# Performance work log

Measured on AMD Instinct MI355X. Metric: run time of the kernel, lower is better.

## Reference

```python
import jax, jax.numpy as jnp
from jax import lax
import numpy as np

DIM = 384
H = W = 32
B = 32
HALF = DIM // 2


def _parc(x, pe, w, b, axis):
    """Global circular depthwise conv along `axis` (2=H, 3=W). w: (C,1,kh,kw)."""
    x = x + pe
    k = x.shape[axis]
    if axis == 2:
        x_cat = jnp.concatenate([x, x[:, :, : k - 1, :]], axis=2)
    else:
        x_cat = jnp.concatenate([x, x[:, :, :, : k - 1]], axis=3)
    out = lax.conv_general_dilated(
        x_cat, w, window_strides=(1, 1), padding='VALID',
        dimension_numbers=('NCHW', 'OIHW', 'NCHW'),
        feature_group_count=x.shape[1])
    return out + b[None, :, None, None]


def setup_inputs() -> dict:
    key = jax.random.key(0)
    ks = jax.random.split(key, 12)
    std = 0.02
    return {
        'x': jax.random.normal(ks[0], (B, DIM, H, W), jnp.float32),
        'pe_h': std * jax.random.normal(ks[1], (1, HALF, H, 1), jnp.float32),
        'w_h': std * jax.random.normal(ks[2], (HALF, 1, H, 1), jnp.float32),
        'b_h': jnp.zeros((HALF,), jnp.float32),
        'pe_w': std * jax.random.normal(ks[3], (1, HALF, 1, W), jnp.float32),
        'w_w': std * jax.random.normal(ks[4], (HALF, 1, 1, W), jnp.float32),
        'b_w': jnp.zeros((HALF,), jnp.float32),
        'ln_w': jnp.ones((DIM,), jnp.float32),
        'ln_b': jnp.zeros((DIM,), jnp.float32),
        'w1': std * jax.random.normal(ks[5], (DIM, 4 * DIM), jnp.float32),
        'b1': jnp.zeros((4 * DIM,), jnp.float32),
        'w2': std * jax.random.normal(ks[6], (4 * DIM, DIM), jnp.float32),
        'b2': jnp.zeros((DIM,), jnp.float32),
        'gamma': 1e-6 * jnp.ones((DIM,), jnp.float32),
    }


def reference(x, pe_h, w_h, b_h, pe_w, w_w, b_w, ln_w, ln_b, w1, b1, w2, b2, gamma):
    inp = x
    half = x.shape[1] // 2
    x_h = _parc(x[:, :half], pe_h, w_h, b_h, axis=2)
    x_w = _parc(x[:, half:], pe_w, w_w, b_w, axis=3)
    y = jnp.concatenate([x_h, x_w], axis=1).transpose(0, 2, 3, 1)  # NHWC
    # LayerNorm over channels (eps=1e-6)
    mu = y.mean(-1, keepdims=True)
    var = ((y - mu) ** 2).mean(-1, keepdims=True)
    y = (y - mu) / jnp.sqrt(var + 1e-6) * ln_w + ln_b
    # inverted MLP: dim -> 4*dim -> dim with exact GELU
    y = jax.nn.gelu(jnp.dot(y, w1) + b1, approximate=False)
    y = jnp.dot(y, w2) + b2
    y = gamma * y
    return inp + y.transpose(0, 3, 1, 2)
```

## Files before the change

kernel.cpp:

```cpp
#include <hip/hip_runtime.h>


typedef __attribute__((ext_vector_type(8))) short short8;
typedef __attribute__((ext_vector_type(4))) float f32x4;
typedef __attribute__((ext_vector_type(16))) float f32x16;
typedef __attribute__((ext_vector_type(4))) int int4v;
typedef __attribute__((ext_vector_type(8))) int i32x8;

__device__ __forceinline__ float bf2f(unsigned short u) {
  union { unsigned int i; float f; } v; v.i = ((unsigned int)u) << 16; return v.f;
}
__device__ __forceinline__ unsigned short f2bf(float f) {
  union { float f; unsigned int i; } v; v.f = f;
  unsigned int r = v.i + 0x7FFFu + ((v.i >> 16) & 1u);
  return (unsigned short)(r >> 16);
}

#if defined(__has_builtin)
#if __has_builtin(__builtin_amdgcn_global_load_lds)
#define HAS_GLL 1
#endif
#endif
#ifndef HAS_GLL
#define HAS_GLL 0
#endif

#if HAS_GLL
__device__ __forceinline__ void gload16(const void* g, void* l) {
  __builtin_amdgcn_global_load_lds((const __attribute__((address_space(1))) void*)g,
                                   (__attribute__((address_space(3))) void*)l, 16, 0, 0);
}
#else
__device__ __forceinline__ void gload16(const void* g, void* l) {
  *(f32x4*)l = *(const f32x4*)g;
}
#endif

template <int N>
__device__ __forceinline__ void wait_vm() {
  asm volatile("s_waitcnt vmcnt(%0)" :: "n"(N) : "memory");
}
__device__ __forceinline__ void barrier_raw() {
  __builtin_amdgcn_s_barrier();
  __builtin_amdgcn_sched_barrier(0);
}

__device__ __forceinline__ float fast_gelu(float h) {
  const float e = __builtin_amdgcn_exp2f(-2.4554005f * h);
  return h * __builtin_amdgcn_rcpf(1.f + e);
}

__device__ __forceinline__ int pk4(float a, float b, float c, float d) {
  int r = __builtin_amdgcn_cvt_pk_fp8_f32(a, b, 0, false);
  return __builtin_amdgcn_cvt_pk_fp8_f32(c, d, r, true);
}

#define SCL1 0x7F7F7F7F

__global__ __launch_bounds__(256) void pack_kernel(
    const float* __restrict__ w1, const float* __restrict__ w2,
    char* __restrict__ w1p, char* __restrict__ w2p) {
  const int t = threadIdx.x;
  const int bid = blockIdx.x;
  float v[64];
  if (bid < 36) {
    const int kt = bid % 6, hg = bid / 6;
    const int h = hg * 256 + t;
    #pragma unroll
    for (int k = 0; k < 64; ++k) v[k] = w1[(size_t)(kt * 64 + k) * 1536 + h];
    const int swz = (h >> 1) & 3;
    char* rowp = w1p + ((size_t)(kt * 1536 + h)) * 64;
    #pragma unroll
    for (int k0 = 0; k0 < 64; k0 += 4) {
      const int chunk = (k0 >> 4) ^ swz;
      *(int*)(rowp + chunk * 16 + (k0 & 12)) = pk4(v[k0], v[k0 + 1], v[k0 + 2], v[k0 + 3]);
    }
  } else {
    const int kt = bid - 36;
    for (int c = t; c < 384; c += 256) {
      #pragma unroll
      for (int k = 0; k < 64; ++k) v[k] = w2[(size_t)(kt * 64 + k) * 384 + c];
      const int swz = (c >> 1) & 3;
      char* rowp = w2p + ((size_t)(kt * 384 + c)) * 64;
      #pragma unroll
      for (int k0 = 0; k0 < 64; k0 += 4) {
        const int chunk = (k0 >> 4) ^ swz;
        *(int*)(rowp + chunk * 16 + (k0 & 12)) = pk4(v[k0], v[k0 + 1], v[k0 + 2], v[k0 + 3]);
      }
    }
  }
}

__global__ __launch_bounds__(256) void conv_kernel(
    const float* __restrict__ x,
    const float* __restrict__ pe_h, const float* __restrict__ w_h, const float* __restrict__ b_h,
    const float* __restrict__ pe_w, const float* __restrict__ w_w, const float* __restrict__ b_w,
    unsigned short* __restrict__ convout) {
  __shared__ float wt_s[8][32], pe_s[8][32], pc_s[8][32];
  const int t = threadIdx.x;
  const int bid = blockIdx.x;
  const int b = bid / 48, g = bid % 48;
  const int c0 = g << 3;
  const bool ish = (c0 < 192);
  const int cl = t >> 5, q = t & 31;
  {
    const int c = c0 + cl;
    if (ish) { wt_s[cl][q] = w_h[(c << 5) + q];           pe_s[cl][q] = pe_h[(c << 5) + q]; }
    else     { const int cc = c - 192;
               wt_s[cl][q] = w_w[(cc << 5) + q];          pe_s[cl][q] = pe_w[(cc << 5) + q]; }
  }
  __syncthreads();
  {
    float s = ish ? b_h[c0 + cl] : b_w[c0 + cl - 192];
    #pragma unroll
    for (int i = 0; i < 32; ++i) s += pe_s[cl][(q + i) & 31] * wt_s[cl][i];
    pc_s[cl][q] = s;
  }
  __syncthreads();
  const float* xp = x + ((size_t)(b * 384 + c0 + cl) << 10);
  float col[32];
  if (ish) {
    #pragma unroll
    for (int j = 0; j < 32; ++j) col[j] = xp[(j << 5) + q];
  } else {
    const float* rp = xp + (q << 5);
    #pragma unroll
    for (int j4 = 0; j4 < 8; ++j4) {
      f32x4 v = *(const f32x4*)&rp[j4 << 2];
      col[j4 * 4 + 0] = v[0]; col[j4 * 4 + 1] = v[1];
      col[j4 * 4 + 2] = v[2]; col[j4 * 4 + 3] = v[3];
    }
  }
  float wr[32];
  #pragma unroll
  for (int i = 0; i < 32; ++i) wr[i] = wt_s[cl][i];
  float o[32];
  #pragma unroll
  for (int oo = 0; oo < 32; ++oo) o[oo] = pc_s[cl][oo];
  #pragma unroll
  for (int i = 0; i < 32; ++i)
    #pragma unroll
    for (int oo = 0; oo < 32; ++oo)
      o[oo] = fmaf(col[(oo + i) & 31], wr[i], o[oo]);
  unsigned short* op = convout + ((size_t)(b * 384 + c0 + cl) << 10);
  if (ish) {
    #pragma unroll
    for (int oo = 0; oo < 32; ++oo) op[(oo << 5) + q] = f2bf(o[oo]);
  } else {
    #pragma unroll
    for (int j8 = 0; j8 < 4; ++j8) {
      short8 p;
      #pragma unroll
      for (int j = 0; j < 8; ++j) p[j] = (short)f2bf(o[j8 * 8 + j]);
      *(short8*)&op[(q << 5) + j8 * 8] = p;
    }
  }
}

__global__ __launch_bounds__(256) void ln_stats_kernel(
    const unsigned short* __restrict__ conv,
    float* __restrict__ mu, float* __restrict__ rs) {
  __shared__ float sums[4][64], sqs[4][64];
  const int tid = threadIdx.x;
  const int lane = tid & 63;
  const int w = tid >> 6;
  const int px = blockIdx.x * 64 + lane;
  const int b = px >> 10, hw = px & 1023;
  const unsigned short* cp = conv + (((size_t)(b * 384 + w * 96)) << 10) + hw;
  float s = 0.f, ss = 0.f;
  #pragma unroll 8
  for (int k = 0; k < 96; ++k) {
    float v = bf2f(cp[(size_t)k << 10]);
    s += v; ss = fmaf(v, v, ss);
  }
  sums[w][lane] = s; sqs[w][lane] = ss;
  __syncthreads();
  if (tid < 64) {
    const float st = sums[0][tid] + sums[1][tid] + sums[2][tid] + sums[3][tid];
    const float sst = sqs[0][tid] + sqs[1][tid] + sqs[2][tid] + sqs[3][tid];
    const float m = st * (1.f / 384.f);
    const float var = sst * (1.f / 384.f) - m * m;
    mu[blockIdx.x * 64 + tid] = m;
    rs[blockIdx.x * 64 + tid] = rsqrtf(var + 1e-6f);
  }
}

__global__ __launch_bounds__(256) void ln_pack_kernel(
    const unsigned short* __restrict__ conv,
    const float* __restrict__ mu, const float* __restrict__ rs,
    char* __restrict__ ylnp,
    const float* __restrict__ ln_w, const float* __restrict__ ln_b) {
  __shared__ float lw[64], lb[64];
  const int kt = blockIdx.y;
  const int t = threadIdx.x;
  if (t < 64) { lw[t] = ln_w[kt * 64 + t]; lb[t] = ln_b[kt * 64 + t]; }
  __syncthreads();
  const int px = blockIdx.x * 256 + t;
  const int b = px >> 10, hw = px & 1023;
  const unsigned short* cp = conv + (((size_t)(b * 384 + kt * 64)) << 10) + hw;
  const float m = mu[px], r = rs[px];
  float ov[64];
  #pragma unroll
  for (int k = 0; k < 64; ++k) {
    const float v = bf2f(cp[(size_t)k << 10]);
    ov[k] = (v - m) * r * lw[k] + lb[k];
  }
  const int swz = (px >> 1) & 3;
  char* rowp = ylnp + ((size_t)(kt * 32768 + px)) * 64;
  #pragma unroll
  for (int q = 0; q < 4; ++q) {
    int4v d;
    d[0] = pk4(ov[q * 16 + 0],  ov[q * 16 + 1],  ov[q * 16 + 2],  ov[q * 16 + 3]);
    d[1] = pk4(ov[q * 16 + 4],  ov[q * 16 + 5],  ov[q * 16 + 6],  ov[q * 16 + 7]);
    d[2] = pk4(ov[q * 16 + 8],  ov[q * 16 + 9],  ov[q * 16 + 10], ov[q * 16 + 11]);
    d[3] = pk4(ov[q * 16 + 12], ov[q * 16 + 13], ov[q * 16 + 14], ov[q * 16 + 15]);
    *(int4v*)(rowp + ((q ^ swz) << 4)) = d;
  }
}

template <int EPI, int KDIM, int AROWS>
__global__ __launch_bounds__(256, 3) void gemm_kernel(
    const char* __restrict__ Ab, const char* __restrict__ Bb,
    char* __restrict__ Hout8, const float* __restrict__ bias,
    const float* __restrict__ gamma, const float* __restrict__ xres,
    float* __restrict__ out, int px0, int bstride, int boff, int hstride,
    int nwg, int nx) {
  extern __shared__ char lds[];
  constexpr int BM = 128, BN = 128;
  constexpr int NB = 3, DEPTH = 2;
  constexpr int NT = KDIM / 64;
  constexpr int SLOT = (BM + BN) * 64;
  constexpr int CH = 4;
  const int tid = threadIdx.x;
  const int lane = tid & 63;
  const int wid = tid >> 6;
  const int wm = wid >> 1, wn = wid & 1;
  const int lane31 = lane & 31;
  const int kh = lane >> 5;
  const int bid = blockIdx.x;
  const int q = nwg >> 3, r = nwg & 7;
  const int xcd = bid & 7, idx = bid >> 3;
  const int lg = (xcd < r ? xcd * (q + 1) : r * (q + 1) + (xcd - r) * q) + idx;
  const int xb = lg % nx, yb = lg / nx;
  const int arow0 = xb * BM;
  const int brow0 = yb * BN;

  f32x16 acc[2][2] = {};

  int aoff[2][2], boffl[2][2];
  #pragma unroll
  for (int m = 0; m < 2; ++m) {
    const int row = wm * 64 + m * 32 + lane31;
    const int s = (row >> 1) & 3;
    aoff[m][0] = row * 64 + (((2 * kh + 0) ^ s) << 4);
    aoff[m][1] = row * 64 + (((2 * kh + 1) ^ s) << 4);
  }
  #pragma unroll
  for (int n = 0; n < 2; ++n) {
    const int row = wn * 64 + n * 32 + lane31;
    const int s = (row >> 1) & 3;
    boffl[n][0] = BM * 64 + row * 64 + (((2 * kh + 0) ^ s) << 4);
    boffl[n][1] = BM * 64 + row * 64 + (((2 * kh + 1) ^ s) << 4);
  }

  auto stage = [&](int tile) {
    char* sl = lds + (size_t)(tile % NB) * SLOT;
    #pragma unroll
    for (int i = 0; i < 2; ++i) {
      const int c = i * 256 + tid;
      const int row = c >> 2, ch = c & 3;
      gload16(Ab + ((size_t)(tile * AROWS + arow0 + row)) * 64 + (ch << 4),
              sl + c * 16);
    }
    #pragma unroll
    for (int i = 0; i < 2; ++i) {
      const int c = i * 256 + tid;
      const int row = c >> 2, ch = c & 3;
      gload16(Bb + ((size_t)tile * bstride + boff + brow0 + row) * 64 + (ch << 4),
              sl + (BM * 4 + c) * 16);
    }
  };

  auto step = [&](int t, int stage_tile) {
    const char* slp = lds + (size_t)(t % NB) * SLOT;
    i32x8 av[2], bv[2];
    #pragma unroll
    for (int m = 0; m < 2; ++m) {
      int4v p0 = *(const int4v*)(slp + aoff[m][0]);
      int4v p1 = *(const int4v*)(slp + aoff[m][1]);
      av[m][0] = p0[0]; av[m][1] = p0[1]; av[m][2] = p0[2]; av[m][3] = p0[3];
      av[m][4] = p1[0]; av[m][5] = p1[1]; av[m][6] = p1[2]; av[m][7] = p1[3];
    }
    #pragma unroll
    for (int n = 0; n < 2; ++n) {
      int4v p0 = *(const int4v*)(slp + boffl[n][0]);
      int4v p1 = *(const int4v*)(slp + boffl[n][1]);
      bv[n][0] = p0[0]; bv[n][1] = p0[1]; bv[n][2] = p0[2]; bv[n][3] = p0[3];
      bv[n][4] = p1[0]; bv[n][5] = p1[1]; bv[n][6] = p1[2]; bv[n][7] = p1[3];
    }
    if (stage_tile >= 0) stage(stage_tile);
    __builtin_amdgcn_s_setprio(1);
    #pragma unroll
    for (int m = 0; m < 2; ++m)
      #pragma unroll
      for (int n = 0; n < 2; ++n)
        acc[m][n] = __builtin_amdgcn_mfma_scale_f32_32x32x64_f8f6f4(
            av[m], bv[n], acc[m][n], 0, 0, 0, SCL1, 0, SCL1);
    __builtin_amdgcn_s_setprio(0);
  };

  #pragma unroll
  for (int d = 0; d < DEPTH; ++d) stage(d);
  wait_vm<CH * (DEPTH - 1)>();
  barrier_raw();

  #pragma unroll 3
  for (int t = 0; t < NT - DEPTH; ++t) {
    step(t, t + DEPTH);
    wait_vm<CH * (DEPTH - 1)>();
    barrier_raw();
  }
  step(NT - 2, -1);
  wait_vm<0>();
  barrier_raw();
  step(NT - 1, -1);

  if (EPI == 0) {
    const int kt = (arow0 + wm * 64) >> 6;
    #pragma unroll
    for (int m = 0; m < 2; ++m) {
      #pragma unroll
      for (int G = 0; G < 4; ++G) {
        const int bytepos = m * 32 + 8 * G + 4 * kh;
        const int hg = arow0 + wm * 64 + bytepos;
        const float b0 = bias[hg + 0], b1v = bias[hg + 1];
        const float b2v = bias[hg + 2], b3v = bias[hg + 3];
        const int chunk = bytepos >> 4, sub = bytepos & 15;
        #pragma unroll
        for (int n = 0; n < 2; ++n) {
          const int px = brow0 + wn * 64 + n * 32 + lane31;
          const int d = pk4(fast_gelu(acc[m][n][4 * G + 0] + b0),
                            fast_gelu(acc[m][n][4 * G + 1] + b1v),
                            fast_gelu(acc[m][n][4 * G + 2] + b2v),
                            fast_gelu(acc[m][n][4 * G + 3] + b3v));
          const int pchunk = chunk ^ ((px >> 1) & 3);
          *(int*)(Hout8 + ((size_t)(kt * hstride + px)) * 64 + pchunk * 16 + sub) = d;
        }
      }
    }
  } else {
    #pragma unroll
    for (int m = 0; m < 2; ++m) {
      #pragma unroll
      for (int G = 0; G < 4; ++G) {
        #pragma unroll
        for (int j = 0; j < 4; ++j) {
          const int c = arow0 + wm * 64 + m * 32 + 8 * G + 4 * kh + j;
          const float gv = gamma[c];
          const float bv = bias[c];
          #pragma unroll
          for (int n = 0; n < 2; ++n) {
            const int px = px0 + brow0 + wn * 64 + n * 32 + lane31;
            const int bb = px >> 10, hw = px & 1023;
            const size_t oi = (((size_t)(bb * 384 + c)) << 10) + hw;
            out[oi] = xres[oi] + gv * (acc[m][n][4 * G + j] + bv);
          }
        }
      }
    }
  }
}

extern "C" void kernel_launch(void* const* d_in, const int* in_sizes, int n_in,
                              void* d_out, int out_size, void* d_ws, size_t ws_size,
                              hipStream_t stream) {
  (void)in_sizes; (void)n_in; (void)out_size;
  const float* x     = (const float*)d_in[0];
  const float* pe_h  = (const float*)d_in[1];
  const float* w_h   = (const float*)d_in[2];
  const float* b_h   = (const float*)d_in[3];
  const float* pe_w  = (const float*)d_in[4];
  const float* w_w   = (const float*)d_in[5];
  const float* b_w   = (const float*)d_in[6];
  const float* ln_w  = (const float*)d_in[7];
  const float* ln_b  = (const float*)d_in[8];
  const float* w1    = (const float*)d_in[9];
  const float* b1    = (const float*)d_in[10];
  const float* w2    = (const float*)d_in[11];
  const float* b2    = (const float*)d_in[12];
  const float* gamma = (const float*)d_in[13];
  float* out = (float*)d_out;
  char* ws = (char*)d_ws;

  char*           W1P  = ws;
  char*           W2P  = ws + 589824;
  float*          MU   = (float*)(ws + 1179648);
  float*          RS   = (float*)(ws + 1310720);
  char*           YLNP = ws + 1441792;
  unsigned short* CONV = (unsigned short*)(ws + 14024704);
  char*           HID  = ws + 14024704;

  int G = 32;
  while (G > 2) {
    size_t hid = (size_t)G * 1572864ull;
    size_t need = 14024704ull + (hid > 25165824ull ? hid : 25165824ull);
    if (need <= ws_size) break;
    G -= 2;
  }

  constexpr int LDS = (128 + 128) * 64 * 3;

  pack_kernel<<<dim3(60), dim3(256), 0, stream>>>(w1, w2, W1P, W2P);
  conv_kernel<<<dim3(1536), dim3(256), 0, stream>>>(x, pe_h, w_h, b_h, pe_w, w_w, b_w, CONV);
  ln_stats_kernel<<<dim3(512), dim3(256), 0, stream>>>(CONV, MU, RS);
  ln_pack_kernel<<<dim3(128, 6), dim3(256), 0, stream>>>(CONV, MU, RS, YLNP, ln_w, ln_b);
  for (int i0 = 0; i0 < 32; i0 += G) {
    const int gi = (32 - i0 < G) ? (32 - i0) : G;
    const int Mpx = gi * 1024;
    {
      const int nwg = 12 * (Mpx / 128);
      gemm_kernel<0, 384, 1536><<<dim3(nwg), dim3(256), LDS, stream>>>(
          W1P, YLNP, HID, b1, nullptr, nullptr, nullptr,
          0, 32768, i0 * 1024, Mpx, nwg, 12);
    }
    {
      const int nwg = 3 * (Mpx / 128);
      gemm_kernel<1, 1536, 384><<<dim3(nwg), dim3(256), LDS, stream>>>(
          W2P, HID, nullptr, b2, gamma, x, out, i0 * 1024, Mpx, 0, 0, nwg, 3);
    }
  }
}
```

Measured before the change: 116.7 us.

## Use MFMA-fragment packed layout and 8-wave GEMM workgroups

Packed FP8 operands (weights, LN output, hidden) move from a row-major XOR-swizzled layout to a fragment-ordered layout. Each 32-row group's k-chunks become contiguous, so LDS fragment reads are linear and each thread stages one contiguous 16-byte chunk. The GEMM goes from 256 to 512 threads per workgroup, with each wave owning a 32x64 sub-tile (two MFMAs) instead of 64x64. The aim is to cut LDS bank conflicts and address math and raise wave-level parallelism, at the cost of fewer MFMAs per LDS read and more barrier participants.

```diff
diff --git a/kernel.cpp b/kernel.cpp
--- a/kernel.cpp
+++ b/kernel.cpp
@@ -56,6 +56,10 @@
 }
 
 #define SCL1 0x7F7F7F7F
+
+__device__ __forceinline__ int packed_off(int row, int kc) {
+  return ((row >> 5) << 11) + ((kc & 1) << 10) + ((kc >> 1) << 9) + ((row & 31) << 4);
+}
 
 __global__ __launch_bounds__(256) void pack_kernel(
     const float* __restrict__ w1, const float* __restrict__ w2,
@@ -68,24 +72,22 @@
     const int h = hg * 256 + t;
     #pragma unroll
     for (int k = 0; k < 64; ++k) v[k] = w1[(size_t)(kt * 64 + k) * 1536 + h];
-    const int swz = (h >> 1) & 3;
-    char* rowp = w1p + ((size_t)(kt * 1536 + h)) * 64;
+    char* base = w1p + (size_t)kt * 1536 * 64;
     #pragma unroll
     for (int k0 = 0; k0 < 64; k0 += 4) {
-      const int chunk = (k0 >> 4) ^ swz;
-      *(int*)(rowp + chunk * 16 + (k0 & 12)) = pk4(v[k0], v[k0 + 1], v[k0 + 2], v[k0 + 3]);
+      *(int*)(base + packed_off(h, k0 >> 4) + (k0 & 12)) =
+          pk4(v[k0], v[k0 + 1], v[k0 + 2], v[k0 + 3]);
     }
   } else {
     const int kt = bid - 36;
     for (int c = t; c < 384; c += 256) {
       #pragma unroll
       for (int k = 0; k < 64; ++k) v[k] = w2[(size_t)(kt * 64 + k) * 384 + c];
-      const int swz = (c >> 1) & 3;
-      char* rowp = w2p + ((size_t)(kt * 384 + c)) * 64;
+      char* base = w2p + (size_t)kt * 384 * 64;
       #pragma unroll
       for (int k0 = 0; k0 < 64; k0 += 4) {
-        const int chunk = (k0 >> 4) ^ swz;
-        *(int*)(rowp + chunk * 16 + (k0 & 12)) = pk4(v[k0], v[k0 + 1], v[k0 + 2], v[k0 + 3]);
+        *(int*)(base + packed_off(c, k0 >> 4) + (k0 & 12)) =
+            pk4(v[k0], v[k0 + 1], v[k0 + 2], v[k0 + 3]);
       }
     }
   }
@@ -205,8 +207,7 @@
     const float v = bf2f(cp[(size_t)k << 10]);
     ov[k] = (v - m) * r * lw[k] + lb[k];
   }
-  const int swz = (px >> 1) & 3;
-  char* rowp = ylnp + ((size_t)(kt * 32768 + px)) * 64;
+  char* base = ylnp + (size_t)kt * 32768 * 64;
   #pragma unroll
   for (int q = 0; q < 4; ++q) {
     int4v d;
@@ -214,12 +215,12 @@
     d[1] = pk4(ov[q * 16 + 4],  ov[q * 16 + 5],  ov[q * 16 + 6],  ov[q * 16 + 7]);
     d[2] = pk4(ov[q * 16 + 8],  ov[q * 16 + 9],  ov[q * 16 + 10], ov[q * 16 + 11]);
     d[3] = pk4(ov[q * 16 + 12], ov[q * 16 + 13], ov[q * 16 + 14], ov[q * 16 + 15]);
-    *(int4v*)(rowp + ((q ^ swz) << 4)) = d;
+    *(int4v*)(base + packed_off(px, q)) = d;
   }
 }
 
 template <int EPI, int KDIM, int AROWS>
-__global__ __launch_bounds__(256, 3) void gemm_kernel(
+__global__ __launch_bounds__(512, 4) void gemm_kernel(
     const char* __restrict__ Ab, const char* __restrict__ Bb,
     char* __restrict__ Hout8, const float* __restrict__ bias,
     const float* __restrict__ gamma, const float* __restrict__ xres,
@@ -230,11 +231,12 @@
   constexpr int NB = 3, DEPTH = 2;
   constexpr int NT = KDIM / 64;
   constexpr int SLOT = (BM + BN) * 64;
-  constexpr int CH = 4;
+  constexpr int CH = 2;
   const int tid = threadIdx.x;
   const int lane = tid & 63;
   const int wid = tid >> 6;
-  const int wm = wid >> 1, wn = wid & 1;
+  const int wm = wid >> 1;
+  const int wn = wid & 1;
   const int lane31 = lane & 31;
   const int kh = lane >> 5;
   const int bid = blockIdx.x;
@@ -245,67 +247,40 @@
   const int arow0 = xb * BM;
   const int brow0 = yb * BN;
 
-  f32x16 acc[2][2] = {};
-
-  int aoff[2][2], boffl[2][2];
-  #pragma unroll
-  for (int m = 0; m < 2; ++m) {
-    const int row = wm * 64 + m * 32 + lane31;
-    const int s = (row >> 1) & 3;
-    aoff[m][0] = row * 64 + (((2 * kh + 0) ^ s) << 4);
-    aoff[m][1] = row * 64 + (((2 * kh + 1) ^ s) << 4);
-  }
-  #pragma unroll
-  for (int n = 0; n < 2; ++n) {
-    const int row = wn * 64 + n * 32 + lane31;
-    const int s = (row >> 1) & 3;
-    boffl[n][0] = BM * 64 + row * 64 + (((2 * kh + 0) ^ s) << 4);
-    boffl[n][1] = BM * 64 + row * 64 + (((2 * kh + 1) ^ s) << 4);
-  }
+  f32x16 acc[2] = {};
+
+  const int abase  = (wm << 11) + (kh << 9) + (lane31 << 4);
+  const int bbase0 = BM * 64 + (((wn << 1) + 0) << 11) + (kh << 9) + (lane31 << 4);
+  const int bbase1 = BM * 64 + (((wn << 1) + 1) << 11) + (kh << 9) + (lane31 << 4);
 
   auto stage = [&](int tile) {
-    char* sl = lds + (size_t)(tile % NB) * SLOT;
-    #pragma unroll
-    for (int i = 0; i < 2; ++i) {
-      const int c = i * 256 + tid;
-      const int row = c >> 2, ch = c & 3;
-      gload16(Ab + ((size_t)(tile * AROWS + arow0 + row)) * 64 + (ch << 4),
-              sl + c * 16);
-    }
-    #pragma unroll
-    for (int i = 0; i < 2; ++i) {
-      const int c = i * 256 + tid;
-      const int row = c >> 2, ch = c & 3;
-      gload16(Bb + ((size_t)tile * bstride + boff + brow0 + row) * 64 + (ch << 4),
-              sl + (BM * 4 + c) * 16);
-    }
+    char* sl = lds + (tile % NB) * SLOT;
+    gload16(Ab + ((size_t)tile * AROWS + arow0) * 64 + tid * 16, sl + tid * 16);
+    gload16(Bb + ((size_t)tile * bstride + boff + brow0) * 64 + tid * 16,
+            sl + BM * 64 + tid * 16);
   };
 
   auto step = [&](int t, int stage_tile) {
-    const char* slp = lds + (size_t)(t % NB) * SLOT;
-    i32x8 av[2], bv[2];
-    #pragma unroll
-    for (int m = 0; m < 2; ++m) {
-      int4v p0 = *(const int4v*)(slp + aoff[m][0]);
-      int4v p1 = *(const int4v*)(slp + aoff[m][1]);
-      av[m][0] = p0[0]; av[m][1] = p0[1]; av[m][2] = p0[2]; av[m][3] = p0[3];
-      av[m][4] = p1[0]; av[m][5] = p1[1]; av[m][6] = p1[2]; av[m][7] = p1[3];
-    }
-    #pragma unroll
-    for (int n = 0; n < 2; ++n) {
-      int4v p0 = *(const int4v*)(slp + boffl[n][0]);
-      int4v p1 = *(const int4v*)(slp + boffl[n][1]);
-      bv[n][0] = p0[0]; bv[n][1] = p0[1]; bv[n][2] = p0[2]; bv[n][3] = p0[3];
-      bv[n][4] = p1[0]; bv[n][5] = p1[1]; bv[n][6] = p1[2]; bv[n][7] = p1[3];
-    }
+    const char* slp = lds + (t % NB) * SLOT;
+    int4v a0  = *(const int4v*)(slp + abase);
+    int4v a1  = *(const int4v*)(slp + abase + 1024);
+    int4v b00 = *(const int4v*)(slp + bbase0);
+    int4v b01 = *(const int4v*)(slp + bbase0 + 1024);
+    int4v b10 = *(const int4v*)(slp + bbase1);
+    int4v b11 = *(const int4v*)(slp + bbase1 + 1024);
+    i32x8 av, bv0, bv1;
+    av[0] = a0[0];  av[1] = a0[1];  av[2] = a0[2];  av[3] = a0[3];
+    av[4] = a1[0];  av[5] = a1[1];  av[6] = a1[2];  av[7] = a1[3];
+    bv0[0] = b00[0]; bv0[1] = b00[1]; bv0[2] = b00[2]; bv0[3] = b00[3];
+    bv0[4] = b01[0]; bv0[5] = b01[1]; bv0[6] = b01[2]; bv0[7] = b01[3];
+    bv1[0] = b10[0]; bv1[1] = b10[1]; bv1[2] = b10[2]; bv1[3] = b10[3];
+    bv1[4] = b11[0]; bv1[5] = b11[1]; bv1[6] = b11[2]; bv1[7] = b11[3];
     if (stage_tile >= 0) stage(stage_tile);
     __builtin_amdgcn_s_setprio(1);
-    #pragma unroll
-    for (int m = 0; m < 2; ++m)
-      #pragma unroll
-      for (int n = 0; n < 2; ++n)
-        acc[m][n] = __builtin_amdgcn_mfma_scale_f32_32x32x64_f8f6f4(
-            av[m], bv[n], acc[m][n], 0, 0, 0, SCL1, 0, SCL1);
+    acc[0] = __builtin_amdgcn_mfma_scale_f32_32x32x64_f8f6f4(
+        av, bv0, acc[0], 0, 0, 0, SCL1, 0, SCL1);
+    acc[1] = __builtin_amdgcn_mfma_scale_f32_32x32x64_f8f6f4(
+        av, bv1, acc[1], 0, 0, 0, SCL1, 0, SCL1);
     __builtin_amdgcn_s_setprio(0);
   };
 
@@ -314,7 +289,7 @@
   wait_vm<CH * (DEPTH - 1)>();
   barrier_raw();
 
-  #pragma unroll 3
+  #pragma unroll 1
   for (int t = 0; t < NT - DEPTH; ++t) {
     step(t, t + DEPTH);
     wait_vm<CH * (DEPTH - 1)>();
@@ -326,45 +301,38 @@
   step(NT - 1, -1);
 
   if (EPI == 0) {
-    const int kt = (arow0 + wm * 64) >> 6;
-    #pragma unroll
-    for (int m = 0; m < 2; ++m) {
+    const int kt2 = (arow0 >> 6) + (wm >> 1);
+    #pragma unroll
+    for (int G = 0; G < 4; ++G) {
+      const int hbyte = ((wm & 1) << 5) + 8 * G + 4 * kh;
+      const int hglob = arow0 + (wm << 5) + 8 * G + 4 * kh;
+      const float c0 = bias[hglob + 0], c1 = bias[hglob + 1];
+      const float c2 = bias[hglob + 2], c3 = bias[hglob + 3];
+      const int kc = hbyte >> 4, sub = hbyte & 15;
       #pragma unroll
-      for (int G = 0; G < 4; ++G) {
-        const int bytepos = m * 32 + 8 * G + 4 * kh;
-        const int hg = arow0 + wm * 64 + bytepos;
-        const float b0 = bias[hg + 0], b1v = bias[hg + 1];
-        const float b2v = bias[hg + 2], b3v = bias[hg + 3];
-        const int chunk = bytepos >> 4, sub = bytepos & 15;
+      for (int n = 0; n < 2; ++n) {
+        const int px = brow0 + ((wn << 1) + n) * 32 + lane31;
+        const int d = pk4(fast_gelu(acc[n][4 * G + 0] + c0),
+                          fast_gelu(acc[n][4 * G + 1] + c1),
+                          fast_gelu(acc[n][4 * G + 2] + c2),
+                          fast_gelu(acc[n][4 * G + 3] + c3));
+        *(int*)(Hout8 + (size_t)kt2 * hstride * 64 + packed_off(px, kc) + sub) = d;
+      }
+    }
+  } else {
+    #pragma unroll
+    for (int G = 0; G < 4; ++G) {
+      #pragma unroll
+      for (int j = 0; j < 4; ++j) {
+        const int c = arow0 + (wm << 5) + 8 * G + 4 * kh + j;
+        const float gv = gamma[c];
+        const float bvv = bias[c];
         #pragma unroll
         for (int n = 0; n < 2; ++n) {
-          const int px = brow0 + wn * 64 + n * 32 + lane31;
-          const int d = pk4(fast_gelu(acc[m][n][4 * G + 0] + b0),
-                            fast_gelu(acc[m][n][4 * G + 1] + b1v),
-                            fast_gelu(acc[m][n][4 * G + 2] + b2v),
-                            fast_gelu(acc[m][n][4 * G + 3] + b3v));
-          const int pchunk = chunk ^ ((px >> 1) & 3);
-          *(int*)(Hout8 + ((size_t)(kt * hstride + px)) * 64 + pchunk * 16 + sub) = d;
-        }
-      }
-    }
-  } else {
-    #pragma unroll
-    for (int m = 0; m < 2; ++m) {
-      #pragma unroll
-      for (int G = 0; G < 4; ++G) {
-        #pragma unroll
-        for (int j = 0; j < 4; ++j) {
-          const int c = arow0 + wm * 64 + m * 32 + 8 * G + 4 * kh + j;
-          const float gv = gamma[c];
-          const float bv = bias[c];
-          #pragma unroll
-          for (int n = 0; n < 2; ++n) {
-            const int px = px0 + brow0 + wn * 64 + n * 32 + lane31;
-            const int bb = px >> 10, hw = px & 1023;
-            const size_t oi = (((size_t)(bb * 384 + c)) << 10) + hw;
-            out[oi] = xres[oi] + gv * (acc[m][n][4 * G + j] + bv);
-          }
+          const int px = px0 + brow0 + ((wn << 1) + n) * 32 + lane31;
+          const int bb = px >> 10, hw = px & 1023;
+          const size_t oi = (((size_t)(bb * 384 + c)) << 10) + hw;
+          out[oi] = xres[oi] + gv * (acc[n][4 * G + j] + bvv);
         }
       }
     }
@@ -419,13 +387,13 @@
     const int Mpx = gi * 1024;
     {
       const int nwg = 12 * (Mpx / 128);
-      gemm_kernel<0, 384, 1536><<<dim3(nwg), dim3(256), LDS, stream>>>(
+      gemm_kernel<0, 384, 1536><<<dim3(nwg), dim3(512), LDS, stream>>>(
           W1P, YLNP, HID, b1, nullptr, nullptr, nullptr,
           0, 32768, i0 * 1024, Mpx, nwg, 12);
     }
     {
       const int nwg = 3 * (Mpx / 128);
-      gemm_kernel<1, 1536, 384><<<dim3(nwg), dim3(256), LDS, stream>>>(
+      gemm_kernel<1, 1536, 384><<<dim3(nwg), dim3(512), LDS, stream>>>(
           W2P, HID, nullptr, b2, gamma, x, out, i0 * 1024, Mpx, 0, 0, nwg, 3);
     }
   }
```

Measured after the change: 110.6 us. 5.2% less time.
